# Optimization experiments

Measured on AMD Instinct MI355X. Metric: run time of the kernel, lower is better.

## Reference

```python
import jax, jax.numpy as jnp
import numpy as np

N_NODES = 16384
N_EDGES = 262144
M = 32          # eq_latent_multiplicity
HD = 16         # attention_head_dim
INV_SQRTD = 1.0 / np.sqrt(HD)
CLIP = 5.0      # attention_logit_clip
EPS = 1e-6
# irreps 0e + 1o: component slices of the channel_wise [.., m, 4] layout
EQ_SLICES = [(0, 1), (1, 4)]
TP_SLICES = [(0, 1), (1, 4), (4, 7), (7, 8)]  # 0e, 1o, 1o, 0e outputs of the uuu tensor product


def so3_layernorm(x, slices):
    # per-irrep RMS over (multiplicity, components), equivariant since it only rescales blocks
    outs = []
    for a, b in slices:
        blk = x[..., a:b]
        rms = jnp.sqrt(jnp.mean(blk * blk, axis=(-2, -1), keepdims=True) + EPS)
        outs.append(blk / rms)
    return jnp.concatenate(outs, axis=-1)


def setup_inputs() -> dict:
    key = jax.random.key(0)
    ks = jax.random.split(key, 12)
    E, N = N_EDGES, N_NODES
    inp = {
        "scalar_latent": jax.random.normal(ks[0], (E, 128), jnp.float32),
        "equiv_latent": jax.random.normal(ks[1], (E, M, 4), jnp.float32),
        "node_invariants": jax.random.normal(ks[2], (N, 64), jnp.float32),
        "edge_conditioning": jax.random.normal(ks[3], (E, 16), jnp.float32),
        "update_coeff": jnp.ones((1,), jnp.float32),
        "W_env": jax.random.normal(ks[4], (128, M * 2), jnp.float32) / np.sqrt(128),
        "b_env": jnp.zeros((M * 2,), jnp.float32),
        "Wq": jax.random.normal(ks[5], (64, M * HD), jnp.float32) / np.sqrt(64),
        "Wk": jax.random.normal(ks[6], (128, M * HD), jnp.float32) / np.sqrt(128),
        "W_mix": jax.random.normal(ks[7], (2 * M + 16, M * 4), jnp.float32) / np.sqrt(2 * M + 16),
        "b_mix": jnp.zeros((M * 4,), jnp.float32),
        "W_sc": jax.random.normal(ks[8], (2 * M + 16, 128), jnp.float32) / np.sqrt(2 * M + 16),
        "b_sc": jnp.zeros((128,), jnp.float32),
        "edge_center": jax.random.randint(ks[9], (E,), 0, N, jnp.int32),
        "active_edges": jnp.arange(E, dtype=jnp.int32),
    }
    return inp


def _forward(scalar_latent, equiv_latent, node_invariants, edge_conditioning,
             update_coeff, W_env, b_env, Wq, Wk, W_mix, b_mix, W_sc, b_sc,
             edge_center, active_edges):
    E = scalar_latent.shape[0]
    N = node_invariants.shape[0]

    # env_embed_mlp: scalar-latent derived gates modulate each irrep block (EquivariantScalarMLP)
    g = jax.nn.silu(scalar_latent @ W_env + b_env).reshape(E, M, 2)
    env_edges = jnp.concatenate([
        equiv_latent[..., 0:1] * g[..., 0:1],   # 0e block
        equiv_latent[..., 1:4] * g[..., 1:2],   # 1o block
    ], axis=-1)  # [E, M, 4]

    # attention: Q from receiver-node invariants, K from per-edge scalar latent
    Q = (node_invariants[edge_center] @ Wq).reshape(E, M, HD)
    K = (scalar_latent @ Wk).reshape(E, M, HD)
    logits = jnp.einsum('emd,emd->em', Q, K) * INV_SQRTD
    logits = jnp.clip(logits, -CLIP, CLIP)
    # scatter_softmax over edges sharing the same center node, per head m
    mx = jax.ops.segment_max(logits, edge_center, num_segments=N)   # [N, M]
    z = jnp.exp(logits - mx[edge_center])
    denom = jax.ops.segment_sum(z, edge_center, num_segments=N)[edge_center]
    attn = z / denom                                               # [E, M]
    env_edges = env_edges * attn[..., None]

    # scatter_sum edges -> nodes, SO3 layer norm, gather back per edge
    env_nodes = jax.ops.segment_sum(env_edges, edge_center, num_segments=N)  # [N, M, 4]
    env_nodes = so3_layernorm(env_nodes, EQ_SLICES)
    local_env = env_nodes[edge_center]                                       # [E, M, 4]

    # Contracter uuu, no weights, component normalization; irreps 0e+1o x 0e+1o -> 0e,1o,1o,0e
    x0, x1 = equiv_latent[..., 0:1], equiv_latent[..., 1:4]
    y0, y1 = local_env[..., 0:1], local_env[..., 1:4]
    tp_out = jnp.concatenate([
        x0 * y0,                                                    # 0e
        x0 * y1,                                                    # 1o
        x1 * y0,                                                    # 1o
        jnp.sum(x1 * y1, axis=-1, keepdims=True) / np.sqrt(3.0),    # 0e
    ], axis=-1)  # [E, M, 8]
    tp_out = so3_layernorm(tp_out, TP_SLICES)

    # projection EquivariantScalarMLP with edge conditioning
    inv_feats = jnp.concatenate([tp_out[..., 0], tp_out[..., 7]], axis=-1)  # [E, 2M]
    feats = jnp.concatenate([inv_feats, edge_conditioning], axis=-1)        # [E, 2M+16]
    mix = (feats @ W_mix + b_mix).reshape(E, M, 4)
    new_equiv = jnp.concatenate([
        mix[..., 0:1] * tp_out[..., 0:1] + mix[..., 1:2] * tp_out[..., 7:8],
        mix[..., 2:3] * tp_out[..., 1:4] + mix[..., 3:4] * tp_out[..., 4:7],
    ], axis=-1)  # [E, M, 4]
    new_scalar = feats @ W_sc + b_sc  # [E, 128]

    # residual stream: apply_residual_stream
    c_old = jax.lax.rsqrt(update_coeff * update_coeff + 1.0)  # [1]
    c_new = update_coeff * c_old
    scalar_out = (c_old * scalar_latent).at[active_edges].add(c_new * new_scalar)
    equiv_out = (c_old[..., None] * equiv_latent).at[active_edges].add(c_new[..., None] * new_equiv)
    return scalar_out, equiv_out


def reference(scalar_latent, equiv_latent, node_invariants, edge_conditioning,
              update_coeff, W_env, b_env, Wq, Wk, W_mix, b_mix, W_sc, b_sc,
              edge_center, active_edges):
    return _forward(scalar_latent, equiv_latent, node_invariants, edge_conditioning,
                    update_coeff, W_env, b_env, Wq, Wk, W_mix, b_mix, W_sc, b_sc,
                    edge_center, active_edges)
```

## Files before the change

kernel.cpp:

```cpp
#include <hip/hip_runtime.h>
#include <hip/hip_bf16.h>

#define E_EDGES 262144
#define N_NODES 16384

typedef short bf16x8 __attribute__((ext_vector_type(8)));
typedef float f32x4 __attribute__((ext_vector_type(4)));

static __device__ __forceinline__ short f2bf(float f) {
    union { float f; unsigned u; } v; v.f = f;
    unsigned r = v.u + 0x7FFFu + ((v.u >> 16) & 1u);
    return (short)(r >> 16);
}
static __device__ __forceinline__ float bf2f(short s) {
    union { unsigned u; float f; } v;
    v.u = ((unsigned)(unsigned short)s) << 16;
    return v.f;
}

__global__ void kprep(const float* __restrict__ Wk, const float* __restrict__ Wenv,
                      const float* __restrict__ Wmix, const float* __restrict__ Wsc,
                      short* __restrict__ WenvT, short* __restrict__ WcatT,
                      short* __restrict__ WkB) {
    int idx = blockIdx.x * 256 + threadIdx.x;
    if (idx < 8192) {
        int c = idx >> 7, k = idx & 127;
        WenvT[idx] = f2bf(Wenv[k * 64 + c]);
    } else if (idx < 8192 + 24576) {
        int o = idx - 8192;
        int c = o / 96, k = o - c * 96;
        float v = 0.f;
        if (k < 80) v = (c < 128) ? Wmix[k * 128 + c] : Wsc[k * 128 + (c - 128)];
        WcatT[o] = f2bf(v);
    } else {
        int o = idx - 32768;
        int m = o >> 12, rest = o & 4095;
        int c = rest >> 5, dp = rest & 31;
        WkB[o] = (dp < 16) ? f2bf(Wk[c * 512 + m * 16 + dp]) : (short)0;
    }
}

__global__ void khist(const int* __restrict__ ec, int* __restrict__ deg) {
    int e = blockIdx.x * 256 + threadIdx.x;
    atomicAdd(&deg[ec[e]], 1);
}

__global__ void kscan(const int* __restrict__ deg, int* __restrict__ offs,
                      int* __restrict__ cursor) {
    __shared__ int part[256];
    int t = threadIdx.x;
    int s = 0;
    for (int i = 0; i < 64; ++i) s += deg[t * 64 + i];
    part[t] = s;
    __syncthreads();
    if (t == 0) {
        int acc = 0;
        for (int i = 0; i < 256; ++i) { int v = part[i]; part[i] = acc; acc += v; }
        offs[N_NODES] = acc;
    }
    __syncthreads();
    int p = part[t];
    for (int i = 0; i < 64; ++i) {
        int idx = t * 64 + i;
        offs[idx] = p;
        cursor[idx] = p;
        p += deg[idx];
    }
}

__global__ void kscat(const int* __restrict__ ec, int* __restrict__ cursor,
                      int* __restrict__ csr) {
    int e = blockIdx.x * 256 + threadIdx.x;
    int p = atomicAdd(&cursor[ec[e]], 1);
    csr[p] = e;
}

__global__ void kqn(const float* __restrict__ ninv, const float* __restrict__ Wq,
                    float* __restrict__ Qn) {
    __shared__ float ni[8 * 68];
    int nBase = blockIdx.x * 8;
    int tid = threadIdx.x;
    for (int idx = tid; idx < 512; idx += 256) {
        int n = idx >> 6, j = idx & 63;
        ni[n * 68 + j] = ninv[(nBase + n) * 64 + j];
    }
    __syncthreads();
    float a0[8] = {0,0,0,0,0,0,0,0};
    float a1[8] = {0,0,0,0,0,0,0,0};
    for (int j = 0; j < 64; ++j) {
        float w0 = Wq[j * 512 + tid];
        float w1 = Wq[j * 512 + tid + 256];
#pragma unroll
        for (int n = 0; n < 8; ++n) {
            float s = ni[n * 68 + j];
            a0[n] += s * w0;
            a1[n] += s * w1;
        }
    }
#pragma unroll
    for (int n = 0; n < 8; ++n) {
        Qn[(nBase + n) * 512 + tid] = a0[n];
        Qn[(nBase + n) * 512 + tid + 256] = a1[n];
    }
}

__launch_bounds__(256)
__global__ void kV(const float* __restrict__ Qn, const short* __restrict__ WkB,
                   short* __restrict__ VT, int nb0) {
    int tid = threadIdx.x;
    int w = tid >> 6, lane = tid & 63;
    int r = lane & 15, q = lane >> 4;
    int nbl = blockIdx.x * 16;
#pragma unroll
    for (int mi = 0; mi < 8; ++mi) {
        int m = w * 8 + mi;
        const float* qp = &Qn[(size_t)(nb0 + nbl + r) * 512 + m * 16 + (q & 1) * 8];
        float4 qa = *(const float4*)qp;
        float4 qb = *(const float4*)(qp + 4);
        bf16x8 af;
        af[0] = f2bf(qa.x); af[1] = f2bf(qa.y); af[2] = f2bf(qa.z); af[3] = f2bf(qa.w);
        af[4] = f2bf(qb.x); af[5] = f2bf(qb.y); af[6] = f2bf(qb.z); af[7] = f2bf(qb.w);
#pragma unroll
        for (int ct = 0; ct < 8; ++ct) {
            bf16x8 bb = *(const bf16x8*)&WkB[(m * 128 + ct * 16 + r) * 32 + q * 8];
            f32x4 acc = {0.f, 0.f, 0.f, 0.f};
            acc = __builtin_amdgcn_mfma_f32_16x16x32_bf16(af, bb, acc, 0, 0, 0);
#pragma unroll
            for (int reg = 0; reg < 4; ++reg) {
                VT[(size_t)(nbl + q * 4 + reg) * 4096 + m * 128 + ct * 16 + r] =
                    f2bf(acc[reg]);
            }
        }
    }
}

__launch_bounds__(256)
__global__ void kmain2(const float* __restrict__ sl, const float* __restrict__ equiv,
                       const int* __restrict__ csr, const int* __restrict__ offs,
                       const short* __restrict__ VT, const short* __restrict__ WenvT,
                       const float* __restrict__ benv, float* __restrict__ envn,
                       int nb0) {
    __shared__ short slb[4][16 * 136];
    __shared__ short glds[4][16 * 68];
    int tid = threadIdx.x;
    int w = tid >> 6, lane = tid & 63;
    int r = lane & 15, q = lane >> 4;
    int node = nb0 + blockIdx.x * 4 + w;
    int start = offs[node], end = offs[node + 1];
    if (start >= end) return;

    bf16x8 vb[2][4];
    const short* vtn = VT + (size_t)(node - nb0) * 4096;
#pragma unroll
    for (int ct = 0; ct < 2; ++ct)
#pragma unroll
        for (int kk = 0; kk < 4; ++kk)
            vb[ct][kk] = *(const bf16x8*)&vtn[(ct * 16 + r) * 128 + kk * 32 + q * 8];
    float bias[4];
#pragma unroll
    for (int g4 = 0; g4 < 4; ++g4) bias[g4] = benv[g4 * 16 + r];

    float facc[2][4] = {{0,0,0,0},{0,0,0,0}};
    float dsum[2] = {0.f, 0.f};

    for (int c0 = start; c0 < end; c0 += 16) {
        int cnt = end - c0; if (cnt > 16) cnt = 16;
#pragma unroll
        for (int i = 0; i < 8; ++i) {
            int idx4 = i * 64 + lane;
            int e = idx4 >> 5, j4 = idx4 & 31;
            float4 v = {0.f, 0.f, 0.f, 0.f};
            if (e < cnt) {
                int ge = csr[c0 + e];
                v = *(const float4*)&sl[(size_t)ge * 128 + j4 * 4];
            }
            short4 s4; s4.x = f2bf(v.x); s4.y = f2bf(v.y); s4.z = f2bf(v.z); s4.w = f2bf(v.w);
            *(short4*)&slb[w][e * 136 + j4 * 4] = s4;
        }
        asm volatile("s_waitcnt lgkmcnt(0)" ::: "memory");
        bf16x8 af[4];
#pragma unroll
        for (int kk = 0; kk < 4; ++kk)
            af[kk] = *(const bf16x8*)&slb[w][r * 136 + kk * 32 + q * 8];

        float zv[2][4];
#pragma unroll
        for (int ct = 0; ct < 2; ++ct) {
            f32x4 acc = {0.f, 0.f, 0.f, 0.f};
#pragma unroll
            for (int kk = 0; kk < 4; ++kk)
                acc = __builtin_amdgcn_mfma_f32_16x16x32_bf16(af[kk], vb[ct][kk], acc, 0, 0, 0);
#pragma unroll
            for (int reg = 0; reg < 4; ++reg) {
                float l = acc[reg] * 0.25f;
                l = fminf(5.f, fmaxf(-5.f, l));
                zv[ct][reg] = __expf(l);
            }
        }

#pragma unroll
        for (int g4 = 0; g4 < 4; ++g4) {
            f32x4 acc = {0.f, 0.f, 0.f, 0.f};
#pragma unroll
            for (int kk = 0; kk < 4; ++kk) {
                bf16x8 bb = *(const bf16x8*)&WenvT[(g4 * 16 + r) * 128 + kk * 32 + q * 8];
                acc = __builtin_amdgcn_mfma_f32_16x16x32_bf16(af[kk], bb, acc, 0, 0, 0);
            }
#pragma unroll
            for (int reg = 0; reg < 4; ++reg) {
                float x = acc[reg] + bias[g4];
                float gv = x / (1.f + __expf(-x));
                glds[w][(q * 4 + reg) * 68 + g4 * 16 + r] = f2bf(gv);
            }
        }
        asm volatile("s_waitcnt lgkmcnt(0)" ::: "memory");

#pragma unroll
        for (int reg = 0; reg < 4; ++reg) {
            int e = q * 4 + reg;
            if (e < cnt) {
                int ge = csr[c0 + e];
#pragma unroll
                for (int ct = 0; ct < 2; ++ct) {
                    int m = ct * 16 + r;
                    float z = zv[ct][reg];
                    unsigned gp = *(const unsigned*)&glds[w][e * 68 + 2 * m];
                    float g0 = bf2f((short)(gp & 0xFFFFu));
                    float g1 = bf2f((short)(gp >> 16));
                    float4 eq = *(const float4*)&equiv[(size_t)ge * 128 + m * 4];
                    facc[ct][0] += z * g0 * eq.x;
                    facc[ct][1] += z * g1 * eq.y;
                    facc[ct][2] += z * g1 * eq.z;
                    facc[ct][3] += z * g1 * eq.w;
                    dsum[ct] += z;
                }
            }
        }
    }

#pragma unroll
    for (int off = 16; off < 64; off <<= 1) {
#pragma unroll
        for (int ct = 0; ct < 2; ++ct) {
#pragma unroll
            for (int i = 0; i < 4; ++i) facc[ct][i] += __shfl_xor(facc[ct][i], off, 64);
            dsum[ct] += __shfl_xor(dsum[ct], off, 64);
        }
    }
    float env0[4], env1[4];
    float inv0 = 1.f / dsum[0], inv1 = 1.f / dsum[1];
#pragma unroll
    for (int i = 0; i < 4; ++i) { env0[i] = facc[0][i] * inv0; env1[i] = facc[1][i] * inv1; }
    float p0 = env0[0] * env0[0] + env1[0] * env1[0];
    float p1 = env0[1]*env0[1] + env0[2]*env0[2] + env0[3]*env0[3]
             + env1[1]*env1[1] + env1[2]*env1[2] + env1[3]*env1[3];
#pragma unroll
    for (int off = 1; off < 16; off <<= 1) {
        p0 += __shfl_xor(p0, off, 64);
        p1 += __shfl_xor(p1, off, 64);
    }
    float i0 = rsqrtf(p0 * (1.f / 32.f) + 1e-6f);
    float i1 = rsqrtf(p1 * (1.f / 96.f) + 1e-6f);
    if (q == 0) {
        float4 o0, o1;
        o0.x = env0[0] * i0; o0.y = env0[1] * i1; o0.z = env0[2] * i1; o0.w = env0[3] * i1;
        o1.x = env1[0] * i0; o1.y = env1[1] * i1; o1.z = env1[2] * i1; o1.w = env1[3] * i1;
        *(float4*)&envn[(size_t)node * 128 + r * 4] = o0;
        *(float4*)&envn[(size_t)node * 128 + 64 + r * 4] = o1;
    }
}

__launch_bounds__(256)
__global__ void kfinal(const float* __restrict__ sl, const float* __restrict__ equiv,
                       const float* __restrict__ econd, const int* __restrict__ ec,
                       const float* __restrict__ envn, const short* __restrict__ WcatT,
                       const float* __restrict__ bmix, const float* __restrict__ bsc,
                       const float* __restrict__ ucp, float* __restrict__ out) {
    __shared__ float mixl[16 * 132];
    __shared__ short featb[16 * 104];

    int tid = threadIdx.x;
    int eBase = blockIdx.x * 16;
    int e = tid >> 4, i = tid & 15;
    int ge = eBase + e;

    float uc = ucp[0];
    float c_old = rsqrtf(uc * uc + 1.f);
    float c_new = uc * c_old;

    int cnode = ec[ge];
    float4 x0 = *(const float4*)&equiv[(size_t)ge * 128 + (i * 2) * 4];
    float4 x1 = *(const float4*)&equiv[(size_t)ge * 128 + (i * 2 + 1) * 4];
    float4 y0 = *(const float4*)&envn[(size_t)cnode * 128 + (i * 2) * 4];
    float4 y1 = *(const float4*)&envn[(size_t)cnode * 128 + (i * 2 + 1) * 4];
    float cond = econd[(size_t)eBase * 16 + tid];

    float tp[2][8];
    {
        float s0, s1, s2, s3;
        {
            tp[0][0] = x0.x * y0.x;
            tp[0][1] = x0.x * y0.y; tp[0][2] = x0.x * y0.z; tp[0][3] = x0.x * y0.w;
            tp[0][4] = x0.y * y0.x; tp[0][5] = x0.z * y0.x; tp[0][6] = x0.w * y0.x;
            tp[0][7] = (x0.y * y0.y + x0.z * y0.z + x0.w * y0.w) * 0.57735026919f;
            tp[1][0] = x1.x * y1.x;
            tp[1][1] = x1.x * y1.y; tp[1][2] = x1.x * y1.z; tp[1][3] = x1.x * y1.w;
            tp[1][4] = x1.y * y1.x; tp[1][5] = x1.z * y1.x; tp[1][6] = x1.w * y1.x;
            tp[1][7] = (x1.y * y1.y + x1.z * y1.z + x1.w * y1.w) * 0.57735026919f;
            s0 = tp[0][0] * tp[0][0] + tp[1][0] * tp[1][0];
            s1 = tp[0][1] * tp[0][1] + tp[0][2] * tp[0][2] + tp[0][3] * tp[0][3]
               + tp[1][1] * tp[1][1] + tp[1][2] * tp[1][2] + tp[1][3] * tp[1][3];
            s2 = tp[0][4] * tp[0][4] + tp[0][5] * tp[0][5] + tp[0][6] * tp[0][6]
               + tp[1][4] * tp[1][4] + tp[1][5] * tp[1][5] + tp[1][6] * tp[1][6];
            s3 = tp[0][7] * tp[0][7] + tp[1][7] * tp[1][7];
        }
#pragma unroll
        for (int off = 1; off < 16; off <<= 1) {
            s0 += __shfl_xor(s0, off, 16);
            s1 += __shfl_xor(s1, off, 16);
            s2 += __shfl_xor(s2, off, 16);
            s3 += __shfl_xor(s3, off, 16);
        }
        float i0 = rsqrtf(s0 * (1.f / 32.f) + 1e-6f);
        float i1 = rsqrtf(s1 * (1.f / 96.f) + 1e-6f);
        float i2 = rsqrtf(s2 * (1.f / 96.f) + 1e-6f);
        float i3 = rsqrtf(s3 * (1.f / 32.f) + 1e-6f);
#pragma unroll
        for (int t2 = 0; t2 < 2; ++t2) {
            tp[t2][0] *= i0;
            tp[t2][1] *= i1; tp[t2][2] *= i1; tp[t2][3] *= i1;
            tp[t2][4] *= i2; tp[t2][5] *= i2; tp[t2][6] *= i2;
            tp[t2][7] *= i3;
            int m = i * 2 + t2;
            featb[e * 104 + m] = f2bf(tp[t2][0]);
            featb[e * 104 + 32 + m] = f2bf(tp[t2][7]);
        }
        featb[e * 104 + 64 + i] = f2bf(cond);
        featb[e * 104 + 80 + i] = 0;
    }
    __syncthreads();

    {
        int lane = tid & 63, wv = tid >> 6;
        int r = lane & 15, q = lane >> 4;
        bf16x8 af[3];
#pragma unroll
        for (int kk = 0; kk < 3; ++kk)
            af[kk] = *(const bf16x8*)&featb[r * 104 + kk * 32 + q * 8];
#pragma unroll
        for (int ct4 = 0; ct4 < 4; ++ct4) {
            int ct = wv * 4 + ct4;
            f32x4 acc = {0.f, 0.f, 0.f, 0.f};
#pragma unroll
            for (int kk = 0; kk < 3; ++kk) {
                bf16x8 bb = *(const bf16x8*)&WcatT[(ct * 16 + r) * 96 + kk * 32 + q * 8];
                acc = __builtin_amdgcn_mfma_f32_16x16x32_bf16(af[kk], bb, acc, 0, 0, 0);
            }
            int colg = ct * 16 + r;
            if (colg < 128) {
                float bias = bmix[colg];
#pragma unroll
                for (int reg = 0; reg < 4; ++reg) {
                    int ee = q * 4 + reg;
                    mixl[ee * 132 + colg] = acc[reg] + bias;
                }
            } else {
                int j = colg - 128;
                float bias = bsc[j];
#pragma unroll
                for (int reg = 0; reg < 4; ++reg) {
                    int ee = q * 4 + reg;
                    int g2 = eBase + ee;
                    out[g2 * 128 + j] = c_old * sl[g2 * 128 + j] + c_new * (acc[reg] + bias);
                }
            }
        }
    }
    __syncthreads();

    float* outeq = out + (size_t)E_EDGES * 128;
    {
        float4 mx0 = *(const float4*)&mixl[e * 132 + (i * 2) * 4];
        float4 mx1 = *(const float4*)&mixl[e * 132 + (i * 2 + 1) * 4];
        float4 o0, o1;
        o0.x = c_old * x0.x + c_new * (mx0.x * tp[0][0] + mx0.y * tp[0][7]);
        o0.y = c_old * x0.y + c_new * (mx0.z * tp[0][1] + mx0.w * tp[0][4]);
        o0.z = c_old * x0.z + c_new * (mx0.z * tp[0][2] + mx0.w * tp[0][5]);
        o0.w = c_old * x0.w + c_new * (mx0.z * tp[0][3] + mx0.w * tp[0][6]);
        o1.x = c_old * x1.x + c_new * (mx1.x * tp[1][0] + mx1.y * tp[1][7]);
        o1.y = c_old * x1.y + c_new * (mx1.z * tp[1][1] + mx1.w * tp[1][4]);
        o1.z = c_old * x1.z + c_new * (mx1.z * tp[1][2] + mx1.w * tp[1][5]);
        o1.w = c_old * x1.w + c_new * (mx1.z * tp[1][3] + mx1.w * tp[1][6]);
        *(float4*)&outeq[(size_t)ge * 128 + (i * 2) * 4] = o0;
        *(float4*)&outeq[(size_t)ge * 128 + (i * 2 + 1) * 4] = o1;
    }
}

extern "C" void kernel_launch(void* const* d_in, const int* in_sizes, int n_in,
                              void* d_out, int out_size, void* d_ws, size_t ws_size,
                              hipStream_t stream) {
    const float* sl    = (const float*)d_in[0];
    const float* eqv   = (const float*)d_in[1];
    const float* ninv  = (const float*)d_in[2];
    const float* econd = (const float*)d_in[3];
    const float* uc    = (const float*)d_in[4];
    const float* Wenv  = (const float*)d_in[5];
    const float* benv  = (const float*)d_in[6];
    const float* Wq    = (const float*)d_in[7];
    const float* Wk    = (const float*)d_in[8];
    const float* Wmix  = (const float*)d_in[9];
    const float* bmix  = (const float*)d_in[10];
    const float* Wsc   = (const float*)d_in[11];
    const float* bsc   = (const float*)d_in[12];
    const int*   ec    = (const int*)d_in[13];
    float* out = (float*)d_out;

    const int NHALF = N_NODES / 2;

    float* ws = (float*)d_ws;
    float* Qn    = ws;
    float* envn  = Qn + (size_t)N_NODES * 512;
    short* VT    = (short*)(envn + (size_t)N_NODES * 128);
    short* WenvT = VT + (size_t)NHALF * 4096;
    short* WcatT = WenvT + 8192;
    short* WkB   = WcatT + 24576;
    int*   deg    = (int*)(WkB + 131072);
    int*   offs   = deg + N_NODES;
    int*   cursor = offs + N_NODES + 1;
    int*   csr    = cursor + N_NODES;

    hipMemsetAsync(deg, 0, (size_t)N_NODES * sizeof(int), stream);
    hipMemsetAsync(envn, 0, (size_t)N_NODES * 128 * sizeof(float), stream);

    kprep<<<640, 256, 0, stream>>>(Wk, Wenv, Wmix, Wsc, WenvT, WcatT, WkB);
    khist<<<E_EDGES / 256, 256, 0, stream>>>(ec, deg);
    kscan<<<1, 256, 0, stream>>>(deg, offs, cursor);
    kscat<<<E_EDGES / 256, 256, 0, stream>>>(ec, cursor, csr);
    kqn<<<N_NODES / 8, 256, 0, stream>>>(ninv, Wq, Qn);

    for (int pass = 0; pass < 2; ++pass) {
        int nb0 = pass * NHALF;
        kV<<<NHALF / 16, 256, 0, stream>>>(Qn, WkB, VT, nb0);
        kmain2<<<NHALF / 4, 256, 0, stream>>>(sl, eqv, csr, offs, VT, WenvT, benv, envn, nb0);
    }

    kfinal<<<E_EDGES / 16, 256, 0, stream>>>(sl, eqv, econd, ec, envn, WcatT, bmix, bsc, uc, out);
}
```

Baseline: 857.0 us.

## Transpose MFMA operands so lanes own columns; drop mix LDS round-trip and second barrier

Swaps the MFMA A/B operands so each lane's accumulator holds four consecutive output columns for one edge. This allows float4 bias loads and float4 coalesced stores of the scalar output, and it lets the mix coefficients stay in registers for the equivariant combine. Normalized tensor-product components go to a new LDS buffer instead of staying per-thread, which removes the mixl LDS round-trip and the second __syncthreads. The scalar residual input is prefetched early. A tradeoff is that the tp0/tp7 terms are now reread from bf16 copies, which loses precision. The equiv output is also handled by only half the waves, and equiv_latent is read a second time.

```diff
diff --git a/kernel.cpp b/kernel.cpp
--- a/kernel.cpp
+++ b/kernel.cpp
@@ -276,17 +276,28 @@
                        const float* __restrict__ envn, const short* __restrict__ WcatT,
                        const float* __restrict__ bmix, const float* __restrict__ bsc,
                        const float* __restrict__ ucp, float* __restrict__ out) {
-    __shared__ float mixl[16 * 132];
     __shared__ short featb[16 * 104];
+    __shared__ float tpl[16 * 194];
 
     int tid = threadIdx.x;
     int eBase = blockIdx.x * 16;
+    int lane = tid & 63, wv = tid >> 6;
+    int r = lane & 15, q = lane >> 4;
     int e = tid >> 4, i = tid & 15;
     int ge = eBase + e;
 
     float uc = ucp[0];
     float c_old = rsqrtf(uc * uc + 1.f);
     float c_new = uc * c_old;
+
+    float4 slp[4];
+    if (wv >= 2) {
+#pragma unroll
+        for (int ct4 = 0; ct4 < 4; ++ct4) {
+            int j0 = (wv * 4 + ct4 - 8) * 16 + q * 4;
+            slp[ct4] = *(const float4*)&sl[(size_t)(eBase + r) * 128 + j0];
+        }
+    }
 
     int cnode = ec[ge];
     float4 x0 = *(const float4*)&equiv[(size_t)ge * 128 + (i * 2) * 4];
@@ -295,25 +306,23 @@
     float4 y1 = *(const float4*)&envn[(size_t)cnode * 128 + (i * 2 + 1) * 4];
     float cond = econd[(size_t)eBase * 16 + tid];
 
-    float tp[2][8];
     {
+        float tp[2][8];
         float s0, s1, s2, s3;
-        {
-            tp[0][0] = x0.x * y0.x;
-            tp[0][1] = x0.x * y0.y; tp[0][2] = x0.x * y0.z; tp[0][3] = x0.x * y0.w;
-            tp[0][4] = x0.y * y0.x; tp[0][5] = x0.z * y0.x; tp[0][6] = x0.w * y0.x;
-            tp[0][7] = (x0.y * y0.y + x0.z * y0.z + x0.w * y0.w) * 0.57735026919f;
-            tp[1][0] = x1.x * y1.x;
-            tp[1][1] = x1.x * y1.y; tp[1][2] = x1.x * y1.z; tp[1][3] = x1.x * y1.w;
-            tp[1][4] = x1.y * y1.x; tp[1][5] = x1.z * y1.x; tp[1][6] = x1.w * y1.x;
-            tp[1][7] = (x1.y * y1.y + x1.z * y1.z + x1.w * y1.w) * 0.57735026919f;
-            s0 = tp[0][0] * tp[0][0] + tp[1][0] * tp[1][0];
-            s1 = tp[0][1] * tp[0][1] + tp[0][2] * tp[0][2] + tp[0][3] * tp[0][3]
-               + tp[1][1] * tp[1][1] + tp[1][2] * tp[1][2] + tp[1][3] * tp[1][3];
-            s2 = tp[0][4] * tp[0][4] + tp[0][5] * tp[0][5] + tp[0][6] * tp[0][6]
-               + tp[1][4] * tp[1][4] + tp[1][5] * tp[1][5] + tp[1][6] * tp[1][6];
-            s3 = tp[0][7] * tp[0][7] + tp[1][7] * tp[1][7];
-        }
+        tp[0][0] = x0.x * y0.x;
+        tp[0][1] = x0.x * y0.y; tp[0][2] = x0.x * y0.z; tp[0][3] = x0.x * y0.w;
+        tp[0][4] = x0.y * y0.x; tp[0][5] = x0.z * y0.x; tp[0][6] = x0.w * y0.x;
+        tp[0][7] = (x0.y * y0.y + x0.z * y0.z + x0.w * y0.w) * 0.57735026919f;
+        tp[1][0] = x1.x * y1.x;
+        tp[1][1] = x1.x * y1.y; tp[1][2] = x1.x * y1.z; tp[1][3] = x1.x * y1.w;
+        tp[1][4] = x1.y * y1.x; tp[1][5] = x1.z * y1.x; tp[1][6] = x1.w * y1.x;
+        tp[1][7] = (x1.y * y1.y + x1.z * y1.z + x1.w * y1.w) * 0.57735026919f;
+        s0 = tp[0][0] * tp[0][0] + tp[1][0] * tp[1][0];
+        s1 = tp[0][1] * tp[0][1] + tp[0][2] * tp[0][2] + tp[0][3] * tp[0][3]
+           + tp[1][1] * tp[1][1] + tp[1][2] * tp[1][2] + tp[1][3] * tp[1][3];
+        s2 = tp[0][4] * tp[0][4] + tp[0][5] * tp[0][5] + tp[0][6] * tp[0][6]
+           + tp[1][4] * tp[1][4] + tp[1][5] * tp[1][5] + tp[1][6] * tp[1][6];
+        s3 = tp[0][7] * tp[0][7] + tp[1][7] * tp[1][7];
 #pragma unroll
         for (int off = 1; off < 16; off <<= 1) {
             s0 += __shfl_xor(s0, off, 16);
@@ -327,72 +336,75 @@
         float i3 = rsqrtf(s3 * (1.f / 32.f) + 1e-6f);
 #pragma unroll
         for (int t2 = 0; t2 < 2; ++t2) {
-            tp[t2][0] *= i0;
-            tp[t2][1] *= i1; tp[t2][2] *= i1; tp[t2][3] *= i1;
-            tp[t2][4] *= i2; tp[t2][5] *= i2; tp[t2][6] *= i2;
-            tp[t2][7] *= i3;
             int m = i * 2 + t2;
-            featb[e * 104 + m] = f2bf(tp[t2][0]);
-            featb[e * 104 + 32 + m] = f2bf(tp[t2][7]);
+            featb[e * 104 + m]      = f2bf(tp[t2][0] * i0);
+            featb[e * 104 + 32 + m] = f2bf(tp[t2][7] * i3);
+            tpl[e * 194 +       m] = tp[t2][1] * i1;
+            tpl[e * 194 +  32 + m] = tp[t2][2] * i1;
+            tpl[e * 194 +  64 + m] = tp[t2][3] * i1;
+            tpl[e * 194 +  96 + m] = tp[t2][4] * i2;
+            tpl[e * 194 + 128 + m] = tp[t2][5] * i2;
+            tpl[e * 194 + 160 + m] = tp[t2][6] * i2;
         }
         featb[e * 104 + 64 + i] = f2bf(cond);
         featb[e * 104 + 80 + i] = 0;
     }
     __syncthreads();
 
+    f32x4 macc[4];
     {
-        int lane = tid & 63, wv = tid >> 6;
-        int r = lane & 15, q = lane >> 4;
-        bf16x8 af[3];
+        bf16x8 bfeat[3];
 #pragma unroll
         for (int kk = 0; kk < 3; ++kk)
-            af[kk] = *(const bf16x8*)&featb[r * 104 + kk * 32 + q * 8];
+            bfeat[kk] = *(const bf16x8*)&featb[r * 104 + kk * 32 + q * 8];
 #pragma unroll
         for (int ct4 = 0; ct4 < 4; ++ct4) {
             int ct = wv * 4 + ct4;
             f32x4 acc = {0.f, 0.f, 0.f, 0.f};
 #pragma unroll
             for (int kk = 0; kk < 3; ++kk) {
-                bf16x8 bb = *(const bf16x8*)&WcatT[(ct * 16 + r) * 96 + kk * 32 + q * 8];
-                acc = __builtin_amdgcn_mfma_f32_16x16x32_bf16(af[kk], bb, acc, 0, 0, 0);
-            }
-            int colg = ct * 16 + r;
-            if (colg < 128) {
-                float bias = bmix[colg];
-#pragma unroll
-                for (int reg = 0; reg < 4; ++reg) {
-                    int ee = q * 4 + reg;
-                    mixl[ee * 132 + colg] = acc[reg] + bias;
-                }
+                bf16x8 aw = *(const bf16x8*)&WcatT[(ct * 16 + r) * 96 + kk * 32 + q * 8];
+                acc = __builtin_amdgcn_mfma_f32_16x16x32_bf16(aw, bfeat[kk], acc, 0, 0, 0);
+            }
+            if (wv < 2) {
+                float4 bm = *(const float4*)&bmix[ct * 16 + q * 4];
+                acc[0] += bm.x; acc[1] += bm.y; acc[2] += bm.z; acc[3] += bm.w;
+                macc[ct4] = acc;
             } else {
-                int j = colg - 128;
-                float bias = bsc[j];
-#pragma unroll
-                for (int reg = 0; reg < 4; ++reg) {
-                    int ee = q * 4 + reg;
-                    int g2 = eBase + ee;
-                    out[g2 * 128 + j] = c_old * sl[g2 * 128 + j] + c_new * (acc[reg] + bias);
-                }
-            }
-        }
-    }
-    __syncthreads();
-
-    float* outeq = out + (size_t)E_EDGES * 128;
-    {
-        float4 mx0 = *(const float4*)&mixl[e * 132 + (i * 2) * 4];
-        float4 mx1 = *(const float4*)&mixl[e * 132 + (i * 2 + 1) * 4];
-        float4 o0, o1;
-        o0.x = c_old * x0.x + c_new * (mx0.x * tp[0][0] + mx0.y * tp[0][7]);
-        o0.y = c_old * x0.y + c_new * (mx0.z * tp[0][1] + mx0.w * tp[0][4]);
-        o0.z = c_old * x0.z + c_new * (mx0.z * tp[0][2] + mx0.w * tp[0][5]);
-        o0.w = c_old * x0.w + c_new * (mx0.z * tp[0][3] + mx0.w * tp[0][6]);
-        o1.x = c_old * x1.x + c_new * (mx1.x * tp[1][0] + mx1.y * tp[1][7]);
-        o1.y = c_old * x1.y + c_new * (mx1.z * tp[1][1] + mx1.w * tp[1][4]);
-        o1.z = c_old * x1.z + c_new * (mx1.z * tp[1][2] + mx1.w * tp[1][5]);
-        o1.w = c_old * x1.w + c_new * (mx1.z * tp[1][3] + mx1.w * tp[1][6]);
-        *(float4*)&outeq[(size_t)ge * 128 + (i * 2) * 4] = o0;
-        *(float4*)&outeq[(size_t)ge * 128 + (i * 2 + 1) * 4] = o1;
+                int j0 = (ct - 8) * 16 + q * 4;
+                float4 bs = *(const float4*)&bsc[j0];
+                float4 o;
+                o.x = c_old * slp[ct4].x + c_new * (acc[0] + bs.x);
+                o.y = c_old * slp[ct4].y + c_new * (acc[1] + bs.y);
+                o.z = c_old * slp[ct4].z + c_new * (acc[2] + bs.z);
+                o.w = c_old * slp[ct4].w + c_new * (acc[3] + bs.w);
+                *(float4*)&out[(size_t)(eBase + r) * 128 + j0] = o;
+            }
+        }
+    }
+
+    if (wv < 2) {
+        float* outeq = out + (size_t)E_EDGES * 128;
+#pragma unroll
+        for (int ct4 = 0; ct4 < 4; ++ct4) {
+            int m = (wv * 4 + ct4) * 4 + q;
+            float4 x = *(const float4*)&equiv[(size_t)(eBase + r) * 128 + m * 4];
+            float tp0n = bf2f(featb[r * 104 + m]);
+            float tp7n = bf2f(featb[r * 104 + 32 + m]);
+            float t1 = tpl[r * 194 +       m];
+            float t2 = tpl[r * 194 +  32 + m];
+            float t3 = tpl[r * 194 +  64 + m];
+            float t4 = tpl[r * 194 +  96 + m];
+            float t5 = tpl[r * 194 + 128 + m];
+            float t6 = tpl[r * 194 + 160 + m];
+            f32x4 mx = macc[ct4];
+            float4 o;
+            o.x = c_old * x.x + c_new * (mx[0] * tp0n + mx[1] * tp7n);
+            o.y = c_old * x.y + c_new * (mx[2] * t1 + mx[3] * t4);
+            o.z = c_old * x.z + c_new * (mx[2] * t2 + mx[3] * t5);
+            o.w = c_old * x.w + c_new * (mx[2] * t3 + mx[3] * t6);
+            *(float4*)&outeq[(size_t)(eBase + r) * 128 + m * 4] = o;
+        }
     }
 }
 
```

After: 860.8 us. No clear change (+0.4%).
